# Performance work log

Hardware: AMD Instinct MI355X
Metric: run time of the kernel (lower is better)

The kernel has to match this reference:

```python
import jax, jax.numpy as jnp
import numpy as np

HIDDEN = 2048
N_HEADS = 16
HEAD_DIM = 128
N_KV_HEADS = 4
MAX_POS = 4096
NEG_INF = -1e9


def _fixed_pos_embedding(features, length):
    # matches generate_fixed_pos_embedding: freqs over arange(0, features, 2)/features
    fraction = jnp.arange(0, features, 2, dtype=jnp.float32) / features
    timescale = 10000.0 ** fraction
    inv_freq = 1.0 / timescale
    sinusoid = jnp.einsum('i,j->ij', jnp.arange(length, dtype=jnp.float32), inv_freq)
    sinusoid = jnp.concatenate([sinusoid, sinusoid], axis=-1)  # [length, features]
    return jnp.sin(sinusoid), jnp.cos(sinusoid)


def setup_inputs() -> dict:
    key = jax.random.key(0)
    k0, k1, k2, k3, k4 = jax.random.split(key, 5)
    B, S = 2, 2048
    hidden_states = jax.random.normal(k0, (B, S, HIDDEN), dtype=jnp.float32)
    # causal additive mask [B,1,S,S]; module forces mask[:, :, :, 0] = 0
    causal = jnp.where(jnp.tril(jnp.ones((S, S), dtype=bool)), 0.0, NEG_INF).astype(jnp.float32)
    causal = causal.at[:, 0].set(0.0)
    attention_mask = jnp.broadcast_to(causal[None, None], (B, 1, S, S))
    std = 0.02
    q_w = jax.random.normal(k1, (N_HEADS * HEAD_DIM, HIDDEN), dtype=jnp.float32) * std
    k_w = jax.random.normal(k2, (N_KV_HEADS * HEAD_DIM, HIDDEN), dtype=jnp.float32) * std
    v_w = jax.random.normal(k3, (N_KV_HEADS * HEAD_DIM, HIDDEN), dtype=jnp.float32) * std
    o_w = jax.random.normal(k4, (HIDDEN, N_HEADS * HEAD_DIM), dtype=jnp.float32) * std
    sin, cos = _fixed_pos_embedding(HEAD_DIM, MAX_POS)
    return {"hidden_states": hidden_states, "attention_mask": attention_mask,
            "q_w": q_w, "k_w": k_w, "v_w": v_w, "o_w": o_w, "sin": sin, "cos": cos}


def _rotate_half(x):
    d = x.shape[-1] // 2
    return jnp.concatenate([-x[..., d:], x[..., :d]], axis=-1)


def reference(hidden_states, attention_mask, q_w, k_w, v_w, o_w, sin, cos):
    B, S, _ = hidden_states.shape
    D = cos.shape[-1]
    H = q_w.shape[0] // D
    KV = k_w.shape[0] // D
    n_rep = H // KV

    # QKV projections (nn.Linear: y = x @ W^T), split into heads: [B,S,h,D]
    q = jnp.einsum('bsh,oh->bso', hidden_states, q_w).reshape(B, S, H, D)
    k = jnp.einsum('bsh,oh->bso', hidden_states, k_w).reshape(B, S, KV, D)
    v = jnp.einsum('bsh,oh->bso', hidden_states, v_w).reshape(B, S, KV, D)

    # rotary embedding (non-decode path: q and k share cos/sin[:S])
    c = cos[:S][None, :, None, :]
    s = sin[:S][None, :, None, :]
    q = q * c + _rotate_half(q) * s
    k = k * c + _rotate_half(k) * s

    # repeat_kv (repeat_interleave along head dim) for GQA
    k = jnp.repeat(k, n_rep, axis=2)  # [B,S,H,D]
    v = jnp.repeat(v, n_rep, axis=2)

    # NOTE: no 1/sqrt(D) scaling -- module uses softmax_scale=1.0
    scores = jnp.einsum('bqhd,bkhd->bhqk', q, k) + attention_mask
    weights = jax.nn.softmax(scores.astype(jnp.float32), axis=-1).astype(q.dtype)
    attn = jnp.einsum('bhqk,bkhd->bqhd', weights, v).reshape(B, S, H * D)
    return jnp.einsum('bso,ho->bsh', attn, o_w)
```

## Files before the change

kernel.cpp:

```cpp
#include <hip/hip_runtime.h>

typedef __bf16 bf16x8 __attribute__((ext_vector_type(8)));
typedef float f32x4 __attribute__((ext_vector_type(4)));

#define LOG2E 1.44269504088896340736f

__device__ __forceinline__ void split16(__bf16* dh, __bf16* dl, const float* src) {
    float4 a[4];
    a[0] = *(const float4*)(src);
    a[1] = *(const float4*)(src + 4);
    a[2] = *(const float4*)(src + 8);
    a[3] = *(const float4*)(src + 12);
    const float* f = (const float*)a;
    bf16x8 h0, h1, l0, l1;
#pragma unroll
    for (int i = 0; i < 8; ++i) {
        float x = f[i];
        __bf16 h = (__bf16)x;
        h0[i] = h; l0[i] = (__bf16)(x - (float)h);
    }
#pragma unroll
    for (int i = 0; i < 8; ++i) {
        float x = f[i + 8];
        __bf16 h = (__bf16)x;
        h1[i] = h; l1[i] = (__bf16)(x - (float)h);
    }
    *(bf16x8*)dh = h0; *(bf16x8*)(dh + 8) = h1;
    *(bf16x8*)dl = l0; *(bf16x8*)(dl + 8) = l1;
}

__global__ __launch_bounds__(256) void gemm_bt_split(
    const float* __restrict__ A, int lda,
    const float* __restrict__ W0, const float* __restrict__ W1,
    const float* __restrict__ W2, int split1, int split2,
    float* __restrict__ C, int K, int ldc)
{
    __shared__ __bf16 Ah[128][48], Al[128][48];
    __shared__ __bf16 Bh[128][48], Bl[128][48];

    const int tid  = threadIdx.x;
    const int lane = tid & 63;
    const int wave = tid >> 6;
    const int m0 = blockIdx.y * 128;
    const int n0 = blockIdx.x * 128;

    const float* W = W0; int wr0 = n0;
    if (n0 >= split2)      { W = W2; wr0 = n0 - split2; }
    else if (n0 >= split1) { W = W1; wr0 = n0 - split1; }

    f32x4 acc[4][4];
    for (int mi = 0; mi < 4; ++mi)
        for (int ni = 0; ni < 4; ++ni)
            acc[mi][ni] = (f32x4){0.f, 0.f, 0.f, 0.f};

    const int srow = tid >> 1;
    const int scol = (tid & 1) * 16;
    const float* aptr = A + (size_t)(m0 + srow) * lda + scol;
    const float* bptr = W + (size_t)(wr0 + srow) * K + scol;

    const int wm = (wave & 1) * 64;
    const int wn = (wave >> 1) * 64;
    const int fr = lane & 15;
    const int fc = (lane >> 4) * 8;
    const int dr = (lane >> 4) * 4;

    for (int k0 = 0; k0 < K; k0 += 32) {
        __syncthreads();
        split16(&Ah[srow][scol], &Al[srow][scol], aptr + k0);
        split16(&Bh[srow][scol], &Bl[srow][scol], bptr + k0);
        __syncthreads();

        bf16x8 afh[4], afl[4], bfh[4], bfl[4];
        for (int i = 0; i < 4; ++i) {
            afh[i] = *(const bf16x8*)&Ah[wm + i * 16 + fr][fc];
            afl[i] = *(const bf16x8*)&Al[wm + i * 16 + fr][fc];
            bfh[i] = *(const bf16x8*)&Bh[wn + i * 16 + fr][fc];
            bfl[i] = *(const bf16x8*)&Bl[wn + i * 16 + fr][fc];
        }
        for (int mi = 0; mi < 4; ++mi)
            for (int ni = 0; ni < 4; ++ni) {
                acc[mi][ni] = __builtin_amdgcn_mfma_f32_16x16x32_bf16(
                    afh[mi], bfh[ni], acc[mi][ni], 0, 0, 0);
                acc[mi][ni] = __builtin_amdgcn_mfma_f32_16x16x32_bf16(
                    afl[mi], bfh[ni], acc[mi][ni], 0, 0, 0);
                acc[mi][ni] = __builtin_amdgcn_mfma_f32_16x16x32_bf16(
                    afh[mi], bfl[ni], acc[mi][ni], 0, 0, 0);
            }
    }

    for (int mi = 0; mi < 4; ++mi)
        for (int ni = 0; ni < 4; ++ni)
            for (int r = 0; r < 4; ++r) {
                int row = m0 + wm + mi * 16 + dr + r;
                int col = n0 + wn + ni * 16 + fr;
                C[(size_t)row * ldc + col] = acc[mi][ni][r];
            }
}

__global__ __launch_bounds__(256) void rope_q(
    float* __restrict__ qkv,
    const float* __restrict__ sinp, const float* __restrict__ cosp)
{
    int t = blockIdx.x * 256 + threadIdx.x;
    int row = t >> 10;
    int rem = t & 1023;
    int col = (rem >> 6) * 128 + (rem & 63);
    int s = row & 2047;
    int d = col & 127;

    float* p = qkv + (size_t)row * 3072 + col;
    float x0  = p[0];
    float x1  = p[64];
    float c0  = cosp[s * 128 + d];
    float c1  = cosp[s * 128 + d + 64];
    float sn0 = sinp[s * 128 + d];
    float sn1 = sinp[s * 128 + d + 64];
    p[0]  = x0 * c0 - x1 * sn0;
    p[64] = x1 * c1 + x0 * sn1;
}

__global__ __launch_bounds__(256) void prep_kv(
    const float* __restrict__ qkv,
    const float* __restrict__ sinp, const float* __restrict__ cosp,
    __bf16* __restrict__ ksp, __bf16* __restrict__ vtsp)
{
    __shared__ float vs[32][132];

    const int tid = threadIdx.x;
    const int kb  = blockIdx.x;
    const int kvh = blockIdx.y;
    const int b   = blockIdx.z;

    {
        const int key = tid >> 1;
        const int dh  = (tid & 1) * 32;
        const int pos = kb * 128 + key;
        const float* src = qkv + (size_t)(b * 2048 + pos) * 3072 + 2048 + kvh * 128;
        __bf16* dst = ksp + ((size_t)((b * 4 + kvh) * 2048) + pos) * 256;
        const float* cp = cosp + pos * 128;
        const float* sp = sinp + pos * 128;
#pragma unroll
        for (int g = 0; g < 4; ++g) {
            int d0 = dh + g * 8;
            float4 x0a = *(const float4*)(src + d0);
            float4 x0b = *(const float4*)(src + d0 + 4);
            float4 x1a = *(const float4*)(src + d0 + 64);
            float4 x1b = *(const float4*)(src + d0 + 68);
            float4 c0a = *(const float4*)(cp + d0);
            float4 c0b = *(const float4*)(cp + d0 + 4);
            float4 c1a = *(const float4*)(cp + d0 + 64);
            float4 c1b = *(const float4*)(cp + d0 + 68);
            float4 s0a = *(const float4*)(sp + d0);
            float4 s0b = *(const float4*)(sp + d0 + 4);
            float4 s1a = *(const float4*)(sp + d0 + 64);
            float4 s1b = *(const float4*)(sp + d0 + 68);
            float x0[8] = {x0a.x,x0a.y,x0a.z,x0a.w,x0b.x,x0b.y,x0b.z,x0b.w};
            float x1[8] = {x1a.x,x1a.y,x1a.z,x1a.w,x1b.x,x1b.y,x1b.z,x1b.w};
            float c0[8] = {c0a.x,c0a.y,c0a.z,c0a.w,c0b.x,c0b.y,c0b.z,c0b.w};
            float c1[8] = {c1a.x,c1a.y,c1a.z,c1a.w,c1b.x,c1b.y,c1b.z,c1b.w};
            float s0[8] = {s0a.x,s0a.y,s0a.z,s0a.w,s0b.x,s0b.y,s0b.z,s0b.w};
            float s1[8] = {s1a.x,s1a.y,s1a.z,s1a.w,s1b.x,s1b.y,s1b.z,s1b.w};
            bf16x8 h0, l0, h1, l1;
#pragma unroll
            for (int i = 0; i < 8; ++i) {
                float y0 = x0[i] * c0[i] - x1[i] * s0[i];
                float y1 = x1[i] * c1[i] + x0[i] * s1[i];
                __bf16 hh0 = (__bf16)y0;
                __bf16 hh1 = (__bf16)y1;
                h0[i] = hh0; l0[i] = (__bf16)(y0 - (float)hh0);
                h1[i] = hh1; l1[i] = (__bf16)(y1 - (float)hh1);
            }
            *(bf16x8*)(dst + d0)            = h0;
            *(bf16x8*)(dst + d0 + 64)       = h1;
            *(bf16x8*)(dst + 128 + d0)      = l0;
            *(bf16x8*)(dst + 128 + d0 + 64) = l1;
        }
    }

    for (int st = 0; st < 4; ++st) {
        __syncthreads();
        {
            const int key = tid >> 3;
            const int dc  = (tid & 7) * 16;
            const float* vsrc = qkv + (size_t)(b * 2048 + kb * 128 + st * 32 + key) * 3072
                                + 2560 + kvh * 128 + dc;
            float4 v0 = *(const float4*)(vsrc);
            float4 v1 = *(const float4*)(vsrc + 4);
            float4 v2 = *(const float4*)(vsrc + 8);
            float4 v3 = *(const float4*)(vsrc + 12);
            *(float4*)&vs[key][dc]      = v0;
            *(float4*)&vs[key][dc + 4]  = v1;
            *(float4*)&vs[key][dc + 8]  = v2;
            *(float4*)&vs[key][dc + 12] = v3;
        }
        __syncthreads();
        {
            const int plane = tid >> 7;
            const int d     = tid & 127;
            bf16x8 ob[4];
#pragma unroll
            for (int k = 0; k < 32; ++k) {
                float x = vs[k][d];
                __bf16 hh = (__bf16)x;
                ob[k >> 3][k & 7] = plane ? (__bf16)(x - (float)hh) : hh;
            }
            __bf16* dst = vtsp + ((((size_t)(b * 4 + kvh) * 64 + kb * 4 + st) * 2 + plane)
                                  * 128 + d) * 32;
            *(bf16x8*)(dst)      = ob[0];
            *(bf16x8*)(dst + 8)  = ob[1];
            *(bf16x8*)(dst + 16) = ob[2];
            *(bf16x8*)(dst + 24) = ob[3];
        }
    }
}

__global__ __launch_bounds__(256, 2) void flash_attn(
    const float* __restrict__ qkv,
    const __bf16* __restrict__ ksp,
    const __bf16* __restrict__ vtsp,
    float* __restrict__ attn)
{
    __shared__ __bf16 Ks[2][32][268];
    __shared__ __bf16 Vt[2][256][34];
    __shared__ float  Psf[4][16][33];

    const int tid  = threadIdx.x;
    const int lane = tid & 63;
    const int wave = tid >> 6;
    const int id   = blockIdx.x;
    const int pair = id & 7;
    const int kvh  = pair & 3;
    const int b    = pair >> 2;
    const int u    = id >> 3;
    const int qb   = (u >> 5) ? (u & 31) : 63 - (u & 31);
    const int h    = kvh * 4 + wave;

    const int fr = lane & 15;
    const int fc = (lane >> 4) * 8;
    const int dr = (lane >> 4) * 4;

    bf16x8 aqh[2][4], aql[2][4];
    for (int rs = 0; rs < 2; ++rs) {
        const size_t qrow = (size_t)(b * 2048 + qb * 32 + rs * 16 + fr) * 3072 + h * 128;
        for (int ks = 0; ks < 4; ++ks) {
            float4 qv[2];
            qv[0] = *(const float4*)(qkv + qrow + ks * 32 + fc);
            qv[1] = *(const float4*)(qkv + qrow + ks * 32 + fc + 4);
            const float* qf = (const float*)qv;
            bf16x8 h8, l8;
#pragma unroll
            for (int i = 0; i < 8; ++i) {
                float x = qf[i];
                __bf16 hh = (__bf16)x;
                h8[i] = hh; l8[i] = (__bf16)(x - (float)hh);
            }
            aqh[rs][ks] = h8; aql[rs][ks] = l8;
        }
    }

    bf16x8 ones;
#pragma unroll
    for (int i = 0; i < 8; ++i) ones[i] = (__bf16)1.0f;

    f32x4 o[2][8];
    for (int rs = 0; rs < 2; ++rs)
        for (int dg = 0; dg < 8; ++dg) o[rs][dg] = (f32x4){0.f, 0.f, 0.f, 0.f};
    f32x4 ls[2] = {(f32x4){0.f,0.f,0.f,0.f}, (f32x4){0.f,0.f,0.f,0.f}};

    const int ntiles = qb + 1;
    const __bf16* kbase = ksp + (size_t)(b * 4 + kvh) * 2048 * 256;
    const __bf16* vbase = vtsp + (size_t)(b * 4 + kvh) * 64 * 8192;

    const int kkey = tid >> 3;
    const int kchk = (tid & 7) * 32;

    for (int kt = 0; kt < ntiles; ++kt) {
        const int buf = kt & 1;
        const int k0 = kt * 32;
        {
            const __bf16* kg = kbase + (size_t)(k0 + kkey) * 256 + kchk;
            bf16x8 v0 = ((const bf16x8*)kg)[0];
            bf16x8 v1 = ((const bf16x8*)kg)[1];
            bf16x8 v2 = ((const bf16x8*)kg)[2];
            bf16x8 v3 = ((const bf16x8*)kg)[3];
            __bf16* d = &Ks[buf][kkey][kchk];
            ((bf16x8*)d)[0] = v0; ((bf16x8*)d)[1] = v1;
            ((bf16x8*)d)[2] = v2; ((bf16x8*)d)[3] = v3;
        }
        {
            const __bf16* vg = vbase + (size_t)kt * 8192 + tid * 32;
            bf16x8 v0 = ((const bf16x8*)vg)[0];
            bf16x8 v1 = ((const bf16x8*)vg)[1];
            bf16x8 v2 = ((const bf16x8*)vg)[2];
            bf16x8 v3 = ((const bf16x8*)vg)[3];
            __bf16* d = &Vt[buf][tid][0];
            ((bf16x8*)d)[0] = v0; ((bf16x8*)d)[1] = v1;
            ((bf16x8*)d)[2] = v2; ((bf16x8*)d)[3] = v3;
        }
        __syncthreads();

        f32x4 s[2][2];
        s[0][0] = s[0][1] = s[1][0] = s[1][1] = (f32x4){0.f, 0.f, 0.f, 0.f};
        for (int ks = 0; ks < 4; ++ks) {
            bf16x8 b0h = *(const bf16x8*)&Ks[buf][fr][ks * 32 + fc];
            bf16x8 b0l = *(const bf16x8*)&Ks[buf][fr][128 + ks * 32 + fc];
            bf16x8 b1h = *(const bf16x8*)&Ks[buf][16 + fr][ks * 32 + fc];
            bf16x8 b1l = *(const bf16x8*)&Ks[buf][16 + fr][128 + ks * 32 + fc];
            for (int rs = 0; rs < 2; ++rs) {
                s[rs][0] = __builtin_amdgcn_mfma_f32_16x16x32_bf16(aqh[rs][ks], b0h, s[rs][0], 0, 0, 0);
                s[rs][0] = __builtin_amdgcn_mfma_f32_16x16x32_bf16(aql[rs][ks], b0h, s[rs][0], 0, 0, 0);
                s[rs][0] = __builtin_amdgcn_mfma_f32_16x16x32_bf16(aqh[rs][ks], b0l, s[rs][0], 0, 0, 0);
                s[rs][1] = __builtin_amdgcn_mfma_f32_16x16x32_bf16(aqh[rs][ks], b1h, s[rs][1], 0, 0, 0);
                s[rs][1] = __builtin_amdgcn_mfma_f32_16x16x32_bf16(aql[rs][ks], b1h, s[rs][1], 0, 0, 0);
                s[rs][1] = __builtin_amdgcn_mfma_f32_16x16x32_bf16(aqh[rs][ks], b1l, s[rs][1], 0, 0, 0);
            }
        }

        bf16x8 ph[2], pl[2];
        for (int rs = 0; rs < 2; ++rs) {
            f32x4 s0 = s[rs][0], s1 = s[rs][1];
            for (int r = 0; r < 4; ++r) {
                int qg = qb * 32 + rs * 16 + dr + r;
                if (k0 + fr > qg)      s0[r] = -1e30f;
                if (k0 + 16 + fr > qg) s1[r] = -1e30f;
                s0[r] = exp2f(s0[r] * LOG2E);
                s1[r] = exp2f(s1[r] * LOG2E);
            }
            for (int r = 0; r < 4; ++r) {
                Psf[wave][dr + r][fr]      = s0[r];
                Psf[wave][dr + r][16 + fr] = s1[r];
            }
            asm volatile("s_waitcnt lgkmcnt(0)" ::: "memory");
            float4 pv[2];
            pv[0] = *(const float4*)&Psf[wave][fr][fc];
            pv[1] = *(const float4*)&Psf[wave][fr][fc + 4];
            asm volatile("s_waitcnt lgkmcnt(0)" ::: "memory");
            const float* pf = (const float*)pv;
#pragma unroll
            for (int i = 0; i < 8; ++i) {
                float x = pf[i];
                __bf16 hh = (__bf16)x;
                ph[rs][i] = hh; pl[rs][i] = (__bf16)(x - (float)hh);
            }
            ls[rs] = __builtin_amdgcn_mfma_f32_16x16x32_bf16(ph[rs], ones, ls[rs], 0, 0, 0);
            ls[rs] = __builtin_amdgcn_mfma_f32_16x16x32_bf16(pl[rs], ones, ls[rs], 0, 0, 0);
        }

        for (int dg = 0; dg < 8; ++dg) {
            bf16x8 bvh = *(const bf16x8*)&Vt[buf][dg * 16 + fr][fc];
            bf16x8 bvl = *(const bf16x8*)&Vt[buf][128 + dg * 16 + fr][fc];
            for (int rs = 0; rs < 2; ++rs) {
                o[rs][dg] = __builtin_amdgcn_mfma_f32_16x16x32_bf16(ph[rs], bvh, o[rs][dg], 0, 0, 0);
                o[rs][dg] = __builtin_amdgcn_mfma_f32_16x16x32_bf16(pl[rs], bvh, o[rs][dg], 0, 0, 0);
                o[rs][dg] = __builtin_amdgcn_mfma_f32_16x16x32_bf16(ph[rs], bvl, o[rs][dg], 0, 0, 0);
            }
        }
    }

    for (int rs = 0; rs < 2; ++rs) {
        const size_t orow = (size_t)(b * 2048 + qb * 32 + rs * 16);
        for (int dg = 0; dg < 8; ++dg)
            for (int r = 0; r < 4; ++r) {
                float val = o[rs][dg][r] / ls[rs][r];
                attn[(orow + dr + r) * 3072 + h * 128 + dg * 16 + fr] = val;
            }
    }
}

extern "C" void kernel_launch(void* const* d_in, const int* in_sizes, int n_in,
                              void* d_out, int out_size, void* d_ws, size_t ws_size,
                              hipStream_t stream)
{
    const float* hs   = (const float*)d_in[0];
    const float* qw   = (const float*)d_in[2];
    const float* kw   = (const float*)d_in[3];
    const float* vw   = (const float*)d_in[4];
    const float* ow   = (const float*)d_in[5];
    const float* sinp = (const float*)d_in[6];
    const float* cosp = (const float*)d_in[7];
    float* outp = (float*)d_out;

    float*  qkv  = (float*)d_ws;
    __bf16* ksp  = (__bf16*)(qkv + (size_t)4096 * 3072);
    __bf16* vtsp = ksp + (size_t)8 * 2048 * 256;
    float*  attn = qkv;

    gemm_bt_split<<<dim3(24, 32), 256, 0, stream>>>(
        hs, 2048, qw, kw, vw, 2048, 2560, qkv, 2048, 3072);
    rope_q<<<16384, 256, 0, stream>>>(qkv, sinp, cosp);
    prep_kv<<<dim3(16, 4, 2), 256, 0, stream>>>(qkv, sinp, cosp, ksp, vtsp);
    flash_attn<<<512, 256, 0, stream>>>(qkv, ksp, vtsp, attn);
    gemm_bt_split<<<dim3(16, 32), 256, 0, stream>>>(
        attn, 3072, ow, ow, ow, 1 << 30, 1 << 30, outp, 2048, 2048);
}
```

Baseline: 673.8 us.

## Pre-split GEMM operands into bf16 planes and load tiles via global_load_lds

The fp32 to hi/lo bf16 splitting moves out of the GEMM inner loop into separate split_matrix kernels for the hidden states and all weights. flash_attn now writes its output directly as bf16 hi/lo planes. The GEMM streams these pre-split tiles straight into LDS with direct global-to-LDS loads instead of converting through registers. The cost is extra launches and workspace, and the weights are re-split on every call. The unpadded LDS rows (stride 32) may also cause bank conflicts when fragments are read.

```diff
diff --git a/kernel.cpp b/kernel.cpp
--- a/kernel.cpp
+++ b/kernel.cpp
@@ -5,38 +5,34 @@
 
 #define LOG2E 1.44269504088896340736f
 
-__device__ __forceinline__ void split16(__bf16* dh, __bf16* dl, const float* src) {
-    float4 a[4];
-    a[0] = *(const float4*)(src);
-    a[1] = *(const float4*)(src + 4);
-    a[2] = *(const float4*)(src + 8);
-    a[3] = *(const float4*)(src + 12);
-    const float* f = (const float*)a;
-    bf16x8 h0, h1, l0, l1;
+#define GLDS16(g, l) __builtin_amdgcn_global_load_lds(                         \
+    (const __attribute__((address_space(1))) unsigned int*)(g),                \
+    (__attribute__((address_space(3))) unsigned int*)(l), 16, 0, 0)
+
+__global__ __launch_bounds__(256) void split_matrix(
+    const float* __restrict__ src, __bf16* __restrict__ dh, __bf16* __restrict__ dl)
+{
+    const size_t t = (size_t)(blockIdx.x * 256 + threadIdx.x) * 8;
+    float4 a = *(const float4*)(src + t);
+    float4 b = *(const float4*)(src + t + 4);
+    float f[8] = {a.x, a.y, a.z, a.w, b.x, b.y, b.z, b.w};
+    bf16x8 h, l;
 #pragma unroll
     for (int i = 0; i < 8; ++i) {
-        float x = f[i];
-        __bf16 h = (__bf16)x;
-        h0[i] = h; l0[i] = (__bf16)(x - (float)h);
-    }
-#pragma unroll
-    for (int i = 0; i < 8; ++i) {
-        float x = f[i + 8];
-        __bf16 h = (__bf16)x;
-        h1[i] = h; l1[i] = (__bf16)(x - (float)h);
-    }
-    *(bf16x8*)dh = h0; *(bf16x8*)(dh + 8) = h1;
-    *(bf16x8*)dl = l0; *(bf16x8*)(dl + 8) = l1;
-}
-
-__global__ __launch_bounds__(256) void gemm_bt_split(
-    const float* __restrict__ A, int lda,
-    const float* __restrict__ W0, const float* __restrict__ W1,
-    const float* __restrict__ W2, int split1, int split2,
+        __bf16 hh = (__bf16)f[i];
+        h[i] = hh; l[i] = (__bf16)(f[i] - (float)hh);
+    }
+    *(bf16x8*)(dh + t) = h;
+    *(bf16x8*)(dl + t) = l;
+}
+
+__global__ __launch_bounds__(256) void gemm_planes(
+    const __bf16* __restrict__ Ah, const __bf16* __restrict__ Al,
+    const __bf16* __restrict__ Bh, const __bf16* __restrict__ Bl,
     float* __restrict__ C, int K, int ldc)
 {
-    __shared__ __bf16 Ah[128][48], Al[128][48];
-    __shared__ __bf16 Bh[128][48], Bl[128][48];
+    __shared__ __bf16 sAh[128 * 32], sAl[128 * 32];
+    __shared__ __bf16 sBh[128 * 32], sBl[128 * 32];
 
     const int tid  = threadIdx.x;
     const int lane = tid & 63;
@@ -44,19 +40,29 @@
     const int m0 = blockIdx.y * 128;
     const int n0 = blockIdx.x * 128;
 
-    const float* W = W0; int wr0 = n0;
-    if (n0 >= split2)      { W = W2; wr0 = n0 - split2; }
-    else if (n0 >= split1) { W = W1; wr0 = n0 - split1; }
+    const int sr  = wave * 32 + (lane >> 2);
+    const int sc  = (lane & 3) * 8;
+    const __bf16* ga0 = Ah + (size_t)(m0 + sr) * K + sc;
+    const __bf16* ga1 = ga0 + (size_t)16 * K;
+    const __bf16* gA0 = Al + (size_t)(m0 + sr) * K + sc;
+    const __bf16* gA1 = gA0 + (size_t)16 * K;
+    const __bf16* gb0 = Bh + (size_t)(n0 + sr) * K + sc;
+    const __bf16* gb1 = gb0 + (size_t)16 * K;
+    const __bf16* gB0 = Bl + (size_t)(n0 + sr) * K + sc;
+    const __bf16* gB1 = gB0 + (size_t)16 * K;
+    __bf16* la0 = &sAh[(wave * 32) * 32];
+    __bf16* la1 = &sAh[(wave * 32 + 16) * 32];
+    __bf16* lA0 = &sAl[(wave * 32) * 32];
+    __bf16* lA1 = &sAl[(wave * 32 + 16) * 32];
+    __bf16* lb0 = &sBh[(wave * 32) * 32];
+    __bf16* lb1 = &sBh[(wave * 32 + 16) * 32];
+    __bf16* lB0 = &sBl[(wave * 32) * 32];
+    __bf16* lB1 = &sBl[(wave * 32 + 16) * 32];
 
     f32x4 acc[4][4];
     for (int mi = 0; mi < 4; ++mi)
         for (int ni = 0; ni < 4; ++ni)
             acc[mi][ni] = (f32x4){0.f, 0.f, 0.f, 0.f};
-
-    const int srow = tid >> 1;
-    const int scol = (tid & 1) * 16;
-    const float* aptr = A + (size_t)(m0 + srow) * lda + scol;
-    const float* bptr = W + (size_t)(wr0 + srow) * K + scol;
 
     const int wm = (wave & 1) * 64;
     const int wn = (wave >> 1) * 64;
@@ -65,19 +71,25 @@
     const int dr = (lane >> 4) * 4;
 
     for (int k0 = 0; k0 < K; k0 += 32) {
+        GLDS16(ga0, la0); GLDS16(ga1, la1);
+        GLDS16(gA0, lA0); GLDS16(gA1, lA1);
+        GLDS16(gb0, lb0); GLDS16(gb1, lb1);
+        GLDS16(gB0, lB0); GLDS16(gB1, lB1);
+        ga0 += 32; ga1 += 32; gA0 += 32; gA1 += 32;
+        gb0 += 32; gb1 += 32; gB0 += 32; gB1 += 32;
         __syncthreads();
-        split16(&Ah[srow][scol], &Al[srow][scol], aptr + k0);
-        split16(&Bh[srow][scol], &Bl[srow][scol], bptr + k0);
-        __syncthreads();
 
         bf16x8 afh[4], afl[4], bfh[4], bfl[4];
+#pragma unroll
         for (int i = 0; i < 4; ++i) {
-            afh[i] = *(const bf16x8*)&Ah[wm + i * 16 + fr][fc];
-            afl[i] = *(const bf16x8*)&Al[wm + i * 16 + fr][fc];
-            bfh[i] = *(const bf16x8*)&Bh[wn + i * 16 + fr][fc];
-            bfl[i] = *(const bf16x8*)&Bl[wn + i * 16 + fr][fc];
-        }
+            afh[i] = *(const bf16x8*)&sAh[(wm + i * 16 + fr) * 32 + fc];
+            afl[i] = *(const bf16x8*)&sAl[(wm + i * 16 + fr) * 32 + fc];
+            bfh[i] = *(const bf16x8*)&sBh[(wn + i * 16 + fr) * 32 + fc];
+            bfl[i] = *(const bf16x8*)&sBl[(wn + i * 16 + fr) * 32 + fc];
+        }
+#pragma unroll
         for (int mi = 0; mi < 4; ++mi)
+#pragma unroll
             for (int ni = 0; ni < 4; ++ni) {
                 acc[mi][ni] = __builtin_amdgcn_mfma_f32_16x16x32_bf16(
                     afh[mi], bfh[ni], acc[mi][ni], 0, 0, 0);
@@ -86,6 +98,7 @@
                 acc[mi][ni] = __builtin_amdgcn_mfma_f32_16x16x32_bf16(
                     afh[mi], bfl[ni], acc[mi][ni], 0, 0, 0);
             }
+        __syncthreads();
     }
 
     for (int mi = 0; mi < 4; ++mi)
@@ -218,7 +231,7 @@
     const float* __restrict__ qkv,
     const __bf16* __restrict__ ksp,
     const __bf16* __restrict__ vtsp,
-    float* __restrict__ attn)
+    __bf16* __restrict__ attnh, __bf16* __restrict__ attnl)
 {
     __shared__ __bf16 Ks[2][32][268];
     __shared__ __bf16 Vt[2][256][34];
@@ -362,7 +375,10 @@
         for (int dg = 0; dg < 8; ++dg)
             for (int r = 0; r < 4; ++r) {
                 float val = o[rs][dg][r] / ls[rs][r];
-                attn[(orow + dr + r) * 3072 + h * 128 + dg * 16 + fr] = val;
+                size_t idx = (orow + dr + r) * 2048 + h * 128 + dg * 16 + fr;
+                __bf16 hh = (__bf16)val;
+                attnh[idx] = hh;
+                attnl[idx] = (__bf16)(val - (float)hh);
             }
     }
 }
@@ -380,16 +396,30 @@
     const float* cosp = (const float*)d_in[7];
     float* outp = (float*)d_out;
 
-    float*  qkv  = (float*)d_ws;
-    __bf16* ksp  = (__bf16*)(qkv + (size_t)4096 * 3072);
-    __bf16* vtsp = ksp + (size_t)8 * 2048 * 256;
-    float*  attn = qkv;
-
-    gemm_bt_split<<<dim3(24, 32), 256, 0, stream>>>(
-        hs, 2048, qw, kw, vw, 2048, 2560, qkv, 2048, 3072);
+    char* w = (char*)d_ws;
+    float*  qkv  = (float*)w;   w += (size_t)4096 * 3072 * 4;
+    __bf16* ksp  = (__bf16*)w;  w += (size_t)8 * 2048 * 256 * 2;
+    __bf16* vtsp = (__bf16*)w;  w += (size_t)8 * 64 * 8192 * 2;
+    __bf16* wqh  = (__bf16*)w;  w += (size_t)3072 * 2048 * 2;
+    __bf16* wql  = (__bf16*)w;  w += (size_t)3072 * 2048 * 2;
+    __bf16* owh  = (__bf16*)w;  w += (size_t)2048 * 2048 * 2;
+    __bf16* owl  = (__bf16*)w;  w += (size_t)2048 * 2048 * 2;
+    __bf16* hsh  = (__bf16*)w;  w += (size_t)4096 * 2048 * 2;
+    __bf16* hsl  = (__bf16*)w;  w += (size_t)4096 * 2048 * 2;
+    __bf16* attnh = hsh;
+    __bf16* attnl = hsl;
+
+    split_matrix<<<4096, 256, 0, stream>>>(hs, hsh, hsl);
+    split_matrix<<<2048, 256, 0, stream>>>(qw, wqh, wql);
+    split_matrix<<<512,  256, 0, stream>>>(kw, wqh + (size_t)2048 * 2048,
+                                               wql + (size_t)2048 * 2048);
+    split_matrix<<<512,  256, 0, stream>>>(vw, wqh + (size_t)2560 * 2048,
+                                               wql + (size_t)2560 * 2048);
+    split_matrix<<<2048, 256, 0, stream>>>(ow, owh, owl);
+
+    gemm_planes<<<dim3(24, 32), 256, 0, stream>>>(hsh, hsl, wqh, wql, qkv, 2048, 3072);
     rope_q<<<16384, 256, 0, stream>>>(qkv, sinp, cosp);
     prep_kv<<<dim3(16, 4, 2), 256, 0, stream>>>(qkv, sinp, cosp, ksp, vtsp);
-    flash_attn<<<512, 256, 0, stream>>>(qkv, ksp, vtsp, attn);
-    gemm_bt_split<<<dim3(16, 32), 256, 0, stream>>>(
-        attn, 3072, ow, ow, ow, 1 << 30, 1 << 30, outp, 2048, 2048);
-}
+    flash_attn<<<512, 256, 0, stream>>>(qkv, ksp, vtsp, attnh, attnl);
+    gemm_planes<<<dim3(16, 32), 256, 0, stream>>>(attnh, attnl, owh, owl, outp, 2048, 2048);
+}
```

Result: faster. 605.9 us (-10.1%).
